# Optimization experiments

Measured on AMD Instinct MI355X. Metric: run time of the kernel, lower is better.

## Reference

```python
import jax, jax.numpy as jnp
import numpy as np

B, N, C, H = 32, 4096, 768, 8
DH = C // H

def setup_inputs() -> dict:
    key = jax.random.key(0)
    k1, k2, k3, k4, k5, k6 = jax.random.split(key, 6)
    s = 0.02
    return {
        "x": jax.random.normal(k1, (B, N, C), dtype=jnp.float32),
        "queries": jax.random.normal(k2, (C,), dtype=jnp.float32),
        "Wq": jax.random.normal(k3, (C, C), dtype=jnp.float32) * s,
        "Wkv": jax.random.normal(k4, (2 * C, C), dtype=jnp.float32) * s,
        "Wproj": jax.random.normal(k5, (C, C), dtype=jnp.float32) * s,
        "bproj": jax.random.normal(k6, (C,), dtype=jnp.float32) * s,
    }

def reference(x, queries, Wq, Wkv, Wproj, bproj):
    # q: single learnable query, shared across batch. torch Linear: y = x @ W^T
    q = (queries @ Wq.T).reshape(H, DH)              # [H, DH]
    kv = jnp.einsum('bnc,ec->bne', x, Wkv)           # [B, N, 2C]
    k, v = jnp.split(kv, 2, axis=-1)
    k = k.reshape(B, N, H, DH)
    v = v.reshape(B, N, H, DH)
    # NOTE: original applies no 1/sqrt(d) scaling
    dots = jnp.einsum('hd,bnhd->bhn', q, k)          # [B, H, N]
    attn = jax.nn.softmax(dots, axis=-1)
    out = jnp.einsum('bhn,bnhd->bhd', attn, v)       # [B, H, DH]
    out = out.reshape(B, 1, C)
    out = jnp.einsum('bnc,ec->bne', out, Wproj) + bproj
    return out                                        # [B, 1, C]
```

## Files before the change

### kernel.cpp

```cpp
#include <hip/hip_runtime.h>

#define B_ 32
#define N_ 4096
#define C_ 768
#define H_ 8
#define DH_ 96
#define TILE 8
#define ROWS 256
#define NT (ROWS / TILE)
#define NCH (N_ / ROWS)
#define TFL (TILE * C_)

struct F3 { float x, y, z; };

#define BARL() do { asm volatile("s_waitcnt lgkmcnt(0)" ::: "memory"); \
                    __builtin_amdgcn_s_barrier(); } while (0)

__global__ __launch_bounds__(256) void k_prep(const float* __restrict__ queries,
    const float* __restrict__ Wq, const float* __restrict__ Wkv,
    float* __restrict__ wqe) {
  __shared__ float qh[DH_];
  const int bid = blockIdx.x;
  const int h = bid / 3, coff = (bid % 3) * 256;
  const int tid = threadIdx.x, lane = tid & 63, wv = tid >> 6;

  float4 q0 = *(const float4*)(queries + lane * 4);
  float4 q1 = *(const float4*)(queries + 256 + lane * 4);
  float4 q2 = *(const float4*)(queries + 512 + lane * 4);
#pragma unroll 4
  for (int j = 0; j < 24; ++j) {
    int d = wv * 24 + j;
    const float* wr = Wq + (size_t)(h * DH_ + d) * C_ + lane * 4;
    float4 w0 = *(const float4*)(wr);
    float4 w1 = *(const float4*)(wr + 256);
    float4 w2 = *(const float4*)(wr + 512);
    float a = w0.x * q0.x;
    a = fmaf(w0.y, q0.y, a); a = fmaf(w0.z, q0.z, a); a = fmaf(w0.w, q0.w, a);
    a = fmaf(w1.x, q1.x, a); a = fmaf(w1.y, q1.y, a);
    a = fmaf(w1.z, q1.z, a); a = fmaf(w1.w, q1.w, a);
    a = fmaf(w2.x, q2.x, a); a = fmaf(w2.y, q2.y, a);
    a = fmaf(w2.z, q2.z, a); a = fmaf(w2.w, q2.w, a);
#pragma unroll
    for (int off = 32; off; off >>= 1) a += __shfl_xor(a, off);
    if (lane == 0) qh[d] = a;
  }
  __syncthreads();

  const int c = coff + tid;
  const float* base = Wkv + (size_t)h * DH_ * C_ + c;
  float a = 0.f;
#pragma unroll 8
  for (int d = 0; d < DH_; ++d)
    a = fmaf(qh[d], base[(size_t)d * C_], a);
  wqe[(size_t)h * C_ + c] = a;
}

__global__ __attribute__((amdgpu_flat_work_group_size(256, 256),
                          amdgpu_waves_per_eu(2, 2))) void k_fused(
    const float* __restrict__ x, const float* __restrict__ wqe,
    float* __restrict__ part, float* __restrict__ sout) {
  extern __shared__ __align__(16) float xdyn[];
  __shared__ __align__(16) float wlds[TILE][H_];
  __shared__ float sden[4][4];

  const int ch = blockIdx.x, b = blockIdx.y;
  const int tid = threadIdx.x, lane = tid & 63, wid = tid >> 6;
  const int rbase = (wid & 1) * 4;
  const int hbase = (wid >> 1) * 4;
  const int col = lane * 4;
  const float* xc = x + ((size_t)b * N_ + (size_t)ch * ROWS) * C_;

  float4 wqv[4][3];
#pragma unroll
  for (int h = 0; h < 4; ++h)
#pragma unroll
    for (int p = 0; p < 3; ++p)
      wqv[h][p] = *(const float4*)(wqe + (size_t)(hbase + h) * C_ + p * 256 + col);

  float acc[H_][3];
#pragma unroll
  for (int h = 0; h < H_; ++h) { acc[h][0] = 0.f; acc[h][1] = 0.f; acc[h][2] = 0.f; }
  float sreg = 0.f;

#define STAGE(BI, T) do {                                                      \
    const float* gt_ = xc + (size_t)(T) * TFL;                                 \
    float* bn_ = xdyn + (size_t)(BI) * TFL;                                    \
    _Pragma("unroll")                                                          \
    for (int j = 0; j < 6; ++j) {                                              \
      int k = wid * 6 + j;                                                     \
      __builtin_amdgcn_global_load_lds(                                        \
        (const __attribute__((address_space(1))) void*)(gt_ + k * 256 + lane * 4), \
        (__attribute__((address_space(3))) void*)(bn_ + k * 256),              \
        16, 0, 0);                                                             \
    }                                                                          \
  } while (0)

  STAGE(0, 0);
  STAGE(1, 1);

  int bi = 0;
  for (int t = 0; t < NT; ++t) {
    if (t < NT - 1) { asm volatile("s_waitcnt vmcnt(6)" ::: "memory"); }
    else           { asm volatile("s_waitcnt vmcnt(0)" ::: "memory"); }
    BARL();
    if (t + 2 < NT) { int nb = bi + 2; if (nb >= 3) nb -= 3; STAGE(nb, t + 2); }
    const float* xb = xdyn + (size_t)bi * TFL;

#pragma unroll
    for (int rr = 0; rr < 4; ++rr) {
      const int r = rbase + rr;
      const float* xr = xb + r * C_ + col;
      float4 xv0 = *(const float4*)(xr);
      float4 xv1 = *(const float4*)(xr + 256);
      float4 xv2 = *(const float4*)(xr + 512);
      float d[4];
#pragma unroll
      for (int h = 0; h < 4; ++h) {
        float a = xv0.x * wqv[h][0].x;
        a = fmaf(xv0.y, wqv[h][0].y, a);
        a = fmaf(xv0.z, wqv[h][0].z, a);
        a = fmaf(xv0.w, wqv[h][0].w, a);
        a = fmaf(xv1.x, wqv[h][1].x, a);
        a = fmaf(xv1.y, wqv[h][1].y, a);
        a = fmaf(xv1.z, wqv[h][1].z, a);
        a = fmaf(xv1.w, wqv[h][1].w, a);
        a = fmaf(xv2.x, wqv[h][2].x, a);
        a = fmaf(xv2.y, wqv[h][2].y, a);
        a = fmaf(xv2.z, wqv[h][2].z, a);
        a = fmaf(xv2.w, wqv[h][2].w, a);
        d[h] = a;
      }
      const int s1 = lane & 1, s2 = lane & 2;
      float A0 = (s1 ? d[1] : d[0]) + __shfl_xor(s1 ? d[0] : d[1], 1);
      float A1 = (s1 ? d[3] : d[2]) + __shfl_xor(s1 ? d[2] : d[3], 1);
      float Q  = (s2 ? A1 : A0) + __shfl_xor(s2 ? A0 : A1, 2);
      Q += __shfl_xor(Q, 4);
      Q += __shfl_xor(Q, 8);
      Q += __shfl_xor(Q, 16);
      Q += __shfl_xor(Q, 32);
      float w = __expf(Q - 20.f);
      if (lane < 4) { wlds[r][hbase + lane] = w; sreg += w; }
    }
    BARL();

    {
      const int c0 = tid * 3;
#pragma unroll
      for (int r = 0; r < TILE; ++r) {
        float4 wA = *(const float4*)(&wlds[r][0]);
        float4 wB = *(const float4*)(&wlds[r][4]);
        F3 xv = *(const F3*)(xb + r * C_ + c0);
        acc[0][0] = fmaf(wA.x, xv.x, acc[0][0]);
        acc[0][1] = fmaf(wA.x, xv.y, acc[0][1]);
        acc[0][2] = fmaf(wA.x, xv.z, acc[0][2]);
        acc[1][0] = fmaf(wA.y, xv.x, acc[1][0]);
        acc[1][1] = fmaf(wA.y, xv.y, acc[1][1]);
        acc[1][2] = fmaf(wA.y, xv.z, acc[1][2]);
        acc[2][0] = fmaf(wA.z, xv.x, acc[2][0]);
        acc[2][1] = fmaf(wA.z, xv.y, acc[2][1]);
        acc[2][2] = fmaf(wA.z, xv.z, acc[2][2]);
        acc[3][0] = fmaf(wA.w, xv.x, acc[3][0]);
        acc[3][1] = fmaf(wA.w, xv.y, acc[3][1]);
        acc[3][2] = fmaf(wA.w, xv.z, acc[3][2]);
        acc[4][0] = fmaf(wB.x, xv.x, acc[4][0]);
        acc[4][1] = fmaf(wB.x, xv.y, acc[4][1]);
        acc[4][2] = fmaf(wB.x, xv.z, acc[4][2]);
        acc[5][0] = fmaf(wB.y, xv.x, acc[5][0]);
        acc[5][1] = fmaf(wB.y, xv.y, acc[5][1]);
        acc[5][2] = fmaf(wB.y, xv.z, acc[5][2]);
        acc[6][0] = fmaf(wB.z, xv.x, acc[6][0]);
        acc[6][1] = fmaf(wB.z, xv.y, acc[6][1]);
        acc[6][2] = fmaf(wB.z, xv.z, acc[6][2]);
        acc[7][0] = fmaf(wB.w, xv.x, acc[7][0]);
        acc[7][1] = fmaf(wB.w, xv.y, acc[7][1]);
        acc[7][2] = fmaf(wB.w, xv.z, acc[7][2]);
      }
    }
    ++bi; if (bi >= 3) bi -= 3;
  }

  {
    const int c0 = tid * 3;
    float* pp = part + ((size_t)(b * NCH + ch) * H_) * C_ + c0;
#pragma unroll
    for (int h = 0; h < H_; ++h) {
      F3 o = { acc[h][0], acc[h][1], acc[h][2] };
      *(F3*)(pp + (size_t)h * C_) = o;
    }
    if (lane < 4) sden[wid][lane] = sreg;
    BARL();
    if (tid < H_) {
      int hh = tid >> 2;
      float den = sden[2 * hh][tid & 3] + sden[2 * hh + 1][tid & 3];
      sout[(size_t)(b * NCH + ch) * H_ + tid] = den;
    }
  }
#undef STAGE
}

__global__ __launch_bounds__(256) void k_combout(
    const float* __restrict__ part, const float* __restrict__ spart,
    const float* __restrict__ Wkv, float* __restrict__ out1) {
  __shared__ __align__(16) float xb[C_];
  const int h = blockIdx.x, b = blockIdx.y;
  const int tid = threadIdx.x, lane = tid & 63, wv = tid >> 6;

  const float* sp = spart + (size_t)b * NCH * H_ + h;
  float den = 0.f;
#pragma unroll
  for (int ch = 0; ch < NCH; ++ch) den += sp[(size_t)ch * H_];
  const float inv = 1.f / den;

  const int c0 = tid * 3;
  const float* pp = part + ((size_t)(b * NCH) * H_ + h) * C_ + c0;
  float a0 = 0.f, a1 = 0.f, a2 = 0.f;
#pragma unroll
  for (int ch = 0; ch < NCH; ++ch) {
    const float* p = pp + (size_t)ch * H_ * C_;
    a0 += p[0]; a1 += p[1]; a2 += p[2];
  }
  xb[c0] = a0 * inv; xb[c0 + 1] = a1 * inv; xb[c0 + 2] = a2 * inv;
  __syncthreads();

  float4 x0 = *(const float4*)(&xb[lane * 4]);
  float4 x1 = *(const float4*)(&xb[256 + lane * 4]);
  float4 x2 = *(const float4*)(&xb[512 + lane * 4]);
#pragma unroll 4
  for (int j = 0; j < 24; ++j) {
    int e = h * DH_ + wv * 24 + j;
    const float* wr = Wkv + (size_t)(C_ + e) * C_ + lane * 4;
    float4 w0 = *(const float4*)(wr);
    float4 w1 = *(const float4*)(wr + 256);
    float4 w2 = *(const float4*)(wr + 512);
    float a = w0.x * x0.x;
    a = fmaf(w0.y, x0.y, a); a = fmaf(w0.z, x0.z, a); a = fmaf(w0.w, x0.w, a);
    a = fmaf(w1.x, x1.x, a); a = fmaf(w1.y, x1.y, a);
    a = fmaf(w1.z, x1.z, a); a = fmaf(w1.w, x1.w, a);
    a = fmaf(w2.x, x2.x, a); a = fmaf(w2.y, x2.y, a);
    a = fmaf(w2.z, x2.z, a); a = fmaf(w2.w, x2.w, a);
#pragma unroll
    for (int off = 32; off; off >>= 1) a += __shfl_xor(a, off);
    if (lane == 0) out1[(size_t)b * C_ + e] = a;
  }
}

__global__ __launch_bounds__(256) void k_proj2(
    const float* __restrict__ out1, const float* __restrict__ Wproj,
    const float* __restrict__ bproj, float* __restrict__ y) {
  __shared__ __align__(16) float xb[C_];
  const int esl = blockIdx.x, b = blockIdx.y;
  const int tid = threadIdx.x, lane = tid & 63, wv = tid >> 6;

  if (tid < 192) ((float4*)xb)[tid] = ((const float4*)(out1 + (size_t)b * C_))[tid];
  __syncthreads();

  float4 x0 = *(const float4*)(&xb[lane * 4]);
  float4 x1 = *(const float4*)(&xb[256 + lane * 4]);
  float4 x2 = *(const float4*)(&xb[512 + lane * 4]);
#pragma unroll 4
  for (int j = 0; j < 24; ++j) {
    int e = esl * DH_ + wv * 24 + j;
    const float* wr = Wproj + (size_t)e * C_ + lane * 4;
    float4 w0 = *(const float4*)(wr);
    float4 w1 = *(const float4*)(wr + 256);
    float4 w2 = *(const float4*)(wr + 512);
    float a = w0.x * x0.x;
    a = fmaf(w0.y, x0.y, a); a = fmaf(w0.z, x0.z, a); a = fmaf(w0.w, x0.w, a);
    a = fmaf(w1.x, x1.x, a); a = fmaf(w1.y, x1.y, a);
    a = fmaf(w1.z, x1.z, a); a = fmaf(w1.w, x1.w, a);
    a = fmaf(w2.x, x2.x, a); a = fmaf(w2.y, x2.y, a);
    a = fmaf(w2.z, x2.z, a); a = fmaf(w2.w, x2.w, a);
#pragma unroll
    for (int off = 32; off; off >>= 1) a += __shfl_xor(a, off);
    if (lane == 0) y[(size_t)b * C_ + e] = a + bproj[e];
  }
}

extern "C" void kernel_launch(void* const* d_in, const int* in_sizes, int n_in,
                              void* d_out, int out_size, void* d_ws, size_t ws_size,
                              hipStream_t stream) {
  const float* x       = (const float*)d_in[0];
  const float* queries = (const float*)d_in[1];
  const float* Wq      = (const float*)d_in[2];
  const float* Wkv     = (const float*)d_in[3];
  const float* Wproj   = (const float*)d_in[4];
  const float* bproj   = (const float*)d_in[5];
  float* y  = (float*)d_out;
  float* ws = (float*)d_ws;

  float* wqe   = ws + 1024;
  float* spart = ws + 8192;
  float* part  = ws + 16384;
  float* out1  = part + (size_t)B_ * NCH * H_ * C_;

  hipLaunchKernelGGL(k_prep,    dim3(24),       dim3(256), 0, stream, queries, Wq, Wkv, wqe);
  hipLaunchKernelGGL(k_fused,   dim3(NCH, B_),  dim3(256),
                     3 * TFL * sizeof(float), stream, x, wqe, part, spart);
  hipLaunchKernelGGL(k_combout, dim3(H_, B_),   dim3(256), 0, stream, part, spart, Wkv, out1);
  hipLaunchKernelGGL(k_proj2,   dim3(H_, B_),   dim3(256), 0, stream, out1, Wproj, bproj, y);
}
```

Measured before the change: 180.1 us.

## Register-prefetch x tiles and compute scores from registers before LDS write

Replaces the triple-buffered global_load_lds pipeline with a register double-buffer: each wave loads its two rows into registers one tile ahead, computes all eight head scores directly from registers, then writes x and weights to a static double-buffered LDS for the weighted accumulation. Each wave now holds all eight head query vectors (96 extra VGPRs) and handles two rows instead of four rows by four heads. This removes one barrier per tile and the LDS read in the score phase, at the cost of much higher register pressure, an extra LDS write pass and only one tile of prefetch depth.

```diff
diff --git a/kernel.cpp b/kernel.cpp
--- a/kernel.cpp
+++ b/kernel.cpp
@@ -59,124 +59,140 @@
                           amdgpu_waves_per_eu(2, 2))) void k_fused(
     const float* __restrict__ x, const float* __restrict__ wqe,
     float* __restrict__ part, float* __restrict__ sout) {
-  extern __shared__ __align__(16) float xdyn[];
-  __shared__ __align__(16) float wlds[TILE][H_];
-  __shared__ float sden[4][4];
+  __shared__ __align__(16) float xsh[2][TFL];
+  __shared__ __align__(16) float wlds[2][TILE][H_];
+  __shared__ float sden[4][H_];
 
   const int ch = blockIdx.x, b = blockIdx.y;
   const int tid = threadIdx.x, lane = tid & 63, wid = tid >> 6;
-  const int rbase = (wid & 1) * 4;
-  const int hbase = (wid >> 1) * 4;
+  const int r0 = wid * 2;
   const int col = lane * 4;
   const float* xc = x + ((size_t)b * N_ + (size_t)ch * ROWS) * C_;
 
-  float4 wqv[4][3];
-#pragma unroll
-  for (int h = 0; h < 4; ++h)
-#pragma unroll
-    for (int p = 0; p < 3; ++p)
-      wqv[h][p] = *(const float4*)(wqe + (size_t)(hbase + h) * C_ + p * 256 + col);
+  float4 wq[3][H_];
+#pragma unroll
+  for (int p = 0; p < 3; ++p)
+#pragma unroll
+    for (int h = 0; h < H_; ++h)
+      wq[p][h] = *(const float4*)(wqe + (size_t)h * C_ + p * 256 + col);
 
   float acc[H_][3];
 #pragma unroll
   for (int h = 0; h < H_; ++h) { acc[h][0] = 0.f; acc[h][1] = 0.f; acc[h][2] = 0.f; }
   float sreg = 0.f;
 
-#define STAGE(BI, T) do {                                                      \
-    const float* gt_ = xc + (size_t)(T) * TFL;                                 \
-    float* bn_ = xdyn + (size_t)(BI) * TFL;                                    \
-    _Pragma("unroll")                                                          \
-    for (int j = 0; j < 6; ++j) {                                              \
-      int k = wid * 6 + j;                                                     \
-      __builtin_amdgcn_global_load_lds(                                        \
-        (const __attribute__((address_space(1))) void*)(gt_ + k * 256 + lane * 4), \
-        (__attribute__((address_space(3))) void*)(bn_ + k * 256),              \
-        16, 0, 0);                                                             \
-    }                                                                          \
+  const int l1 = lane & 1, l2 = (lane >> 1) & 1, l4 = (lane >> 2) & 1;
+
+  float4 stA[6], stB[6];
+
+#define LOADT(DST, T) do {                                                  \
+    const float* gt_ = xc + (size_t)(T) * TFL + (size_t)r0 * C_ + col;      \
+    DST[0] = *(const float4*)(gt_);                                         \
+    DST[1] = *(const float4*)(gt_ + 256);                                   \
+    DST[2] = *(const float4*)(gt_ + 512);                                   \
+    DST[3] = *(const float4*)(gt_ + C_);                                    \
+    DST[4] = *(const float4*)(gt_ + C_ + 256);                              \
+    DST[5] = *(const float4*)(gt_ + C_ + 512);                              \
   } while (0)
 
-  STAGE(0, 0);
-  STAGE(1, 1);
-
-  int bi = 0;
-  for (int t = 0; t < NT; ++t) {
-    if (t < NT - 1) { asm volatile("s_waitcnt vmcnt(6)" ::: "memory"); }
-    else           { asm volatile("s_waitcnt vmcnt(0)" ::: "memory"); }
-    BARL();
-    if (t + 2 < NT) { int nb = bi + 2; if (nb >= 3) nb -= 3; STAGE(nb, t + 2); }
-    const float* xb = xdyn + (size_t)bi * TFL;
-
-#pragma unroll
-    for (int rr = 0; rr < 4; ++rr) {
-      const int r = rbase + rr;
-      const float* xr = xb + r * C_ + col;
-      float4 xv0 = *(const float4*)(xr);
-      float4 xv1 = *(const float4*)(xr + 256);
-      float4 xv2 = *(const float4*)(xr + 512);
-      float d[4];
-#pragma unroll
-      for (int h = 0; h < 4; ++h) {
-        float a = xv0.x * wqv[h][0].x;
-        a = fmaf(xv0.y, wqv[h][0].y, a);
-        a = fmaf(xv0.z, wqv[h][0].z, a);
-        a = fmaf(xv0.w, wqv[h][0].w, a);
-        a = fmaf(xv1.x, wqv[h][1].x, a);
-        a = fmaf(xv1.y, wqv[h][1].y, a);
-        a = fmaf(xv1.z, wqv[h][1].z, a);
-        a = fmaf(xv1.w, wqv[h][1].w, a);
-        a = fmaf(xv2.x, wqv[h][2].x, a);
-        a = fmaf(xv2.y, wqv[h][2].y, a);
-        a = fmaf(xv2.z, wqv[h][2].z, a);
-        a = fmaf(xv2.w, wqv[h][2].w, a);
-        d[h] = a;
-      }
-      const int s1 = lane & 1, s2 = lane & 2;
-      float A0 = (s1 ? d[1] : d[0]) + __shfl_xor(s1 ? d[0] : d[1], 1);
-      float A1 = (s1 ? d[3] : d[2]) + __shfl_xor(s1 ? d[2] : d[3], 1);
-      float Q  = (s2 ? A1 : A0) + __shfl_xor(s2 ? A0 : A1, 2);
-      Q += __shfl_xor(Q, 4);
-      Q += __shfl_xor(Q, 8);
-      Q += __shfl_xor(Q, 16);
-      Q += __shfl_xor(Q, 32);
-      float w = __expf(Q - 20.f);
-      if (lane < 4) { wlds[r][hbase + lane] = w; sreg += w; }
-    }
-    BARL();
-
-    {
-      const int c0 = tid * 3;
-#pragma unroll
-      for (int r = 0; r < TILE; ++r) {
-        float4 wA = *(const float4*)(&wlds[r][0]);
-        float4 wB = *(const float4*)(&wlds[r][4]);
-        F3 xv = *(const F3*)(xb + r * C_ + c0);
-        acc[0][0] = fmaf(wA.x, xv.x, acc[0][0]);
-        acc[0][1] = fmaf(wA.x, xv.y, acc[0][1]);
-        acc[0][2] = fmaf(wA.x, xv.z, acc[0][2]);
-        acc[1][0] = fmaf(wA.y, xv.x, acc[1][0]);
-        acc[1][1] = fmaf(wA.y, xv.y, acc[1][1]);
-        acc[1][2] = fmaf(wA.y, xv.z, acc[1][2]);
-        acc[2][0] = fmaf(wA.z, xv.x, acc[2][0]);
-        acc[2][1] = fmaf(wA.z, xv.y, acc[2][1]);
-        acc[2][2] = fmaf(wA.z, xv.z, acc[2][2]);
-        acc[3][0] = fmaf(wA.w, xv.x, acc[3][0]);
-        acc[3][1] = fmaf(wA.w, xv.y, acc[3][1]);
-        acc[3][2] = fmaf(wA.w, xv.z, acc[3][2]);
-        acc[4][0] = fmaf(wB.x, xv.x, acc[4][0]);
-        acc[4][1] = fmaf(wB.x, xv.y, acc[4][1]);
-        acc[4][2] = fmaf(wB.x, xv.z, acc[4][2]);
-        acc[5][0] = fmaf(wB.y, xv.x, acc[5][0]);
-        acc[5][1] = fmaf(wB.y, xv.y, acc[5][1]);
-        acc[5][2] = fmaf(wB.y, xv.z, acc[5][2]);
-        acc[6][0] = fmaf(wB.z, xv.x, acc[6][0]);
-        acc[6][1] = fmaf(wB.z, xv.y, acc[6][1]);
-        acc[6][2] = fmaf(wB.z, xv.z, acc[6][2]);
-        acc[7][0] = fmaf(wB.w, xv.x, acc[7][0]);
-        acc[7][1] = fmaf(wB.w, xv.y, acc[7][1]);
-        acc[7][2] = fmaf(wB.w, xv.z, acc[7][2]);
-      }
-    }
-    ++bi; if (bi >= 3) bi -= 3;
+#define ROWDOT(V0, V1, V2, WOUT) do {                                       \
+    float d_[H_];                                                           \
+    _Pragma("unroll")                                                       \
+    for (int h = 0; h < H_; ++h) {                                          \
+      float a_ = (V0).x * wq[0][h].x;                                       \
+      a_ = fmaf((V0).y, wq[0][h].y, a_);                                    \
+      a_ = fmaf((V0).z, wq[0][h].z, a_);                                    \
+      a_ = fmaf((V0).w, wq[0][h].w, a_);                                    \
+      a_ = fmaf((V1).x, wq[1][h].x, a_);                                    \
+      a_ = fmaf((V1).y, wq[1][h].y, a_);                                    \
+      a_ = fmaf((V1).z, wq[1][h].z, a_);                                    \
+      a_ = fmaf((V1).w, wq[1][h].w, a_);                                    \
+      a_ = fmaf((V2).x, wq[2][h].x, a_);                                    \
+      a_ = fmaf((V2).y, wq[2][h].y, a_);                                    \
+      a_ = fmaf((V2).z, wq[2][h].z, a_);                                    \
+      a_ = fmaf((V2).w, wq[2][h].w, a_);                                    \
+      d_[h] = a_;                                                           \
+    }                                                                       \
+    float k_, g_;                                                           \
+    k_ = l1 ? d_[1] : d_[0]; g_ = l1 ? d_[0] : d_[1];                       \
+    float q0_ = k_ + __shfl_xor(g_, 1);                                     \
+    k_ = l1 ? d_[3] : d_[2]; g_ = l1 ? d_[2] : d_[3];                       \
+    float q1_ = k_ + __shfl_xor(g_, 1);                                     \
+    k_ = l1 ? d_[5] : d_[4]; g_ = l1 ? d_[4] : d_[5];                       \
+    float q2_ = k_ + __shfl_xor(g_, 1);                                     \
+    k_ = l1 ? d_[7] : d_[6]; g_ = l1 ? d_[6] : d_[7];                       \
+    float q3_ = k_ + __shfl_xor(g_, 1);                                     \
+    k_ = l2 ? q1_ : q0_; g_ = l2 ? q0_ : q1_;                               \
+    float r0_ = k_ + __shfl_xor(g_, 2);                                     \
+    k_ = l2 ? q3_ : q2_; g_ = l2 ? q2_ : q3_;                               \
+    float r1_ = k_ + __shfl_xor(g_, 2);                                     \
+    k_ = l4 ? r1_ : r0_; g_ = l4 ? r0_ : r1_;                               \
+    float t_ = k_ + __shfl_xor(g_, 4);                                      \
+    t_ += __shfl_xor(t_, 8);                                                \
+    t_ += __shfl_xor(t_, 16);                                               \
+    t_ += __shfl_xor(t_, 32);                                               \
+    WOUT = __expf(t_ - 20.f);                                               \
+  } while (0)
+
+#define BODY(T, P, CUR, NXT) do {                                           \
+    if ((T) + 1 < NT) LOADT(NXT, (T) + 1);                                  \
+    if ((T) + 1 < NT) { asm volatile("s_waitcnt vmcnt(6)" ::: "memory"); }  \
+    else              { asm volatile("s_waitcnt vmcnt(0)" ::: "memory"); }  \
+    float wA_, wB_;                                                         \
+    ROWDOT(CUR[0], CUR[1], CUR[2], wA_);                                    \
+    ROWDOT(CUR[3], CUR[4], CUR[5], wB_);                                    \
+    sreg += wA_ + wB_;                                                      \
+    if (lane < H_) {                                                        \
+      wlds[P][r0][lane]     = wA_;                                          \
+      wlds[P][r0 + 1][lane] = wB_;                                          \
+    }                                                                       \
+    { float* bw = &xsh[P][(size_t)r0 * C_];                                 \
+      *(float4*)(bw + col)            = CUR[0];                             \
+      *(float4*)(bw + 256 + col)      = CUR[1];                             \
+      *(float4*)(bw + 512 + col)      = CUR[2];                             \
+      *(float4*)(bw + C_ + col)       = CUR[3];                             \
+      *(float4*)(bw + C_ + 256 + col) = CUR[4];                             \
+      *(float4*)(bw + C_ + 512 + col) = CUR[5];                             \
+    }                                                                       \
+    BARL();                                                                 \
+    { const int c0 = tid * 3;                                               \
+      _Pragma("unroll")                                                     \
+      for (int r = 0; r < TILE; ++r) {                                      \
+        float4 wAv = *(const float4*)(&wlds[P][r][0]);                      \
+        float4 wBv = *(const float4*)(&wlds[P][r][4]);                      \
+        F3 xv = *(const F3*)(&xsh[P][(size_t)r * C_ + c0]);                 \
+        acc[0][0] = fmaf(wAv.x, xv.x, acc[0][0]);                           \
+        acc[0][1] = fmaf(wAv.x, xv.y, acc[0][1]);                           \
+        acc[0][2] = fmaf(wAv.x, xv.z, acc[0][2]);                           \
+        acc[1][0] = fmaf(wAv.y, xv.x, acc[1][0]);                           \
+        acc[1][1] = fmaf(wAv.y, xv.y, acc[1][1]);                           \
+        acc[1][2] = fmaf(wAv.y, xv.z, acc[1][2]);                           \
+        acc[2][0] = fmaf(wAv.z, xv.x, acc[2][0]);                           \
+        acc[2][1] = fmaf(wAv.z, xv.y, acc[2][1]);                           \
+        acc[2][2] = fmaf(wAv.z, xv.z, acc[2][2]);                           \
+        acc[3][0] = fmaf(wAv.w, xv.x, acc[3][0]);                           \
+        acc[3][1] = fmaf(wAv.w, xv.y, acc[3][1]);                           \
+        acc[3][2] = fmaf(wAv.w, xv.z, acc[3][2]);                           \
+        acc[4][0] = fmaf(wBv.x, xv.x, acc[4][0]);                           \
+        acc[4][1] = fmaf(wBv.x, xv.y, acc[4][1]);                           \
+        acc[4][2] = fmaf(wBv.x, xv.z, acc[4][2]);                           \
+        acc[5][0] = fmaf(wBv.y, xv.x, acc[5][0]);                           \
+        acc[5][1] = fmaf(wBv.y, xv.y, acc[5][1]);                           \
+        acc[5][2] = fmaf(wBv.y, xv.z, acc[5][2]);                           \
+        acc[6][0] = fmaf(wBv.z, xv.x, acc[6][0]);                           \
+        acc[6][1] = fmaf(wBv.z, xv.y, acc[6][1]);                           \
+        acc[6][2] = fmaf(wBv.z, xv.z, acc[6][2]);                           \
+        acc[7][0] = fmaf(wBv.w, xv.x, acc[7][0]);                           \
+        acc[7][1] = fmaf(wBv.w, xv.y, acc[7][1]);                           \
+        acc[7][2] = fmaf(wBv.w, xv.z, acc[7][2]);                           \
+      }                                                                     \
+    }                                                                       \
+  } while (0)
+
+  LOADT(stA, 0);
+  for (int t2 = 0; t2 < NT; t2 += 2) {
+    BODY(t2,     0, stA, stB);
+    BODY(t2 + 1, 1, stB, stA);
   }
 
   {
@@ -187,15 +203,16 @@
       F3 o = { acc[h][0], acc[h][1], acc[h][2] };
       *(F3*)(pp + (size_t)h * C_) = o;
     }
-    if (lane < 4) sden[wid][lane] = sreg;
+    if (lane < H_) sden[wid][lane] = sreg;
     BARL();
     if (tid < H_) {
-      int hh = tid >> 2;
-      float den = sden[2 * hh][tid & 3] + sden[2 * hh + 1][tid & 3];
+      float den = sden[0][tid] + sden[1][tid] + sden[2][tid] + sden[3][tid];
       sout[(size_t)(b * NCH + ch) * H_ + tid] = den;
     }
   }
-#undef STAGE
+#undef BODY
+#undef ROWDOT
+#undef LOADT
 }
 
 __global__ __launch_bounds__(256) void k_combout(
@@ -294,8 +311,7 @@
   float* out1  = part + (size_t)B_ * NCH * H_ * C_;
 
   hipLaunchKernelGGL(k_prep,    dim3(24),       dim3(256), 0, stream, queries, Wq, Wkv, wqe);
-  hipLaunchKernelGGL(k_fused,   dim3(NCH, B_),  dim3(256),
-                     3 * TFL * sizeof(float), stream, x, wqe, part, spart);
+  hipLaunchKernelGGL(k_fused,   dim3(NCH, B_),  dim3(256), 0, stream, x, wqe, part, spart);
   hipLaunchKernelGGL(k_combout, dim3(H_, B_),   dim3(256), 0, stream, part, spart, Wkv, out1);
   hipLaunchKernelGGL(k_proj2,   dim3(H_, B_),   dim3(256), 0, stream, out1, Wproj, bproj, y);
 }
```

New measurement: 420.4 us. 134% more time.

## Software-pipeline score and accumulate phases to drop one barrier per tile

Applied to the files above, without the earlier changes.

Restructures the main loop so the weighted-accumulation phase for tile t-1 runs after the score phase of tile t, using double-buffered softmax weights in LDS. This removes the second block barrier per tile. In exchange, global prefetch depth drops from two tiles ahead to one, and every iteration now waits for all outstanding loads (vmcnt(0)), which may expose memory latency.

```diff
diff --git a/kernel.cpp b/kernel.cpp
--- a/kernel.cpp
+++ b/kernel.cpp
@@ -60,7 +60,7 @@
     const float* __restrict__ x, const float* __restrict__ wqe,
     float* __restrict__ part, float* __restrict__ sout) {
   extern __shared__ __align__(16) float xdyn[];
-  __shared__ __align__(16) float wlds[TILE][H_];
+  __shared__ __align__(16) float wlds[2][TILE][H_];
   __shared__ float sden[4][4];
 
   const int ch = blockIdx.x, b = blockIdx.y;
@@ -95,16 +95,49 @@
     }                                                                          \
   } while (0)
 
+#define PHASEC(XB, PC) do {                                                    \
+    const int c0 = tid * 3;                                                    \
+    _Pragma("unroll")                                                          \
+    for (int r = 0; r < TILE; ++r) {                                           \
+      float4 wA = *(const float4*)(&wlds[PC][r][0]);                           \
+      float4 wB = *(const float4*)(&wlds[PC][r][4]);                           \
+      F3 xv = *(const F3*)((XB) + (size_t)r * C_ + c0);                        \
+      acc[0][0] = fmaf(wA.x, xv.x, acc[0][0]);                                 \
+      acc[0][1] = fmaf(wA.x, xv.y, acc[0][1]);                                 \
+      acc[0][2] = fmaf(wA.x, xv.z, acc[0][2]);                                 \
+      acc[1][0] = fmaf(wA.y, xv.x, acc[1][0]);                                 \
+      acc[1][1] = fmaf(wA.y, xv.y, acc[1][1]);                                 \
+      acc[1][2] = fmaf(wA.y, xv.z, acc[1][2]);                                 \
+      acc[2][0] = fmaf(wA.z, xv.x, acc[2][0]);                                 \
+      acc[2][1] = fmaf(wA.z, xv.y, acc[2][1]);                                 \
+      acc[2][2] = fmaf(wA.z, xv.z, acc[2][2]);                                 \
+      acc[3][0] = fmaf(wA.w, xv.x, acc[3][0]);                                 \
+      acc[3][1] = fmaf(wA.w, xv.y, acc[3][1]);                                 \
+      acc[3][2] = fmaf(wA.w, xv.z, acc[3][2]);                                 \
+      acc[4][0] = fmaf(wB.x, xv.x, acc[4][0]);                                 \
+      acc[4][1] = fmaf(wB.x, xv.y, acc[4][1]);                                 \
+      acc[4][2] = fmaf(wB.x, xv.z, acc[4][2]);                                 \
+      acc[5][0] = fmaf(wB.y, xv.x, acc[5][0]);                                 \
+      acc[5][1] = fmaf(wB.y, xv.y, acc[5][1]);                                 \
+      acc[5][2] = fmaf(wB.y, xv.z, acc[5][2]);                                 \
+      acc[6][0] = fmaf(wB.z, xv.x, acc[6][0]);                                 \
+      acc[6][1] = fmaf(wB.z, xv.y, acc[6][1]);                                 \
+      acc[6][2] = fmaf(wB.z, xv.z, acc[6][2]);                                 \
+      acc[7][0] = fmaf(wB.w, xv.x, acc[7][0]);                                 \
+      acc[7][1] = fmaf(wB.w, xv.y, acc[7][1]);                                 \
+      acc[7][2] = fmaf(wB.w, xv.z, acc[7][2]);                                 \
+    }                                                                          \
+  } while (0)
+
   STAGE(0, 0);
-  STAGE(1, 1);
 
   int bi = 0;
   for (int t = 0; t < NT; ++t) {
-    if (t < NT - 1) { asm volatile("s_waitcnt vmcnt(6)" ::: "memory"); }
-    else           { asm volatile("s_waitcnt vmcnt(0)" ::: "memory"); }
+    asm volatile("s_waitcnt vmcnt(0)" ::: "memory");
     BARL();
-    if (t + 2 < NT) { int nb = bi + 2; if (nb >= 3) nb -= 3; STAGE(nb, t + 2); }
+    if (t + 1 < NT) { int nb = bi + 1; if (nb >= 3) nb -= 3; STAGE(nb, t + 1); }
     const float* xb = xdyn + (size_t)bi * TFL;
+    const int P = t & 1;
 
 #pragma unroll
     for (int rr = 0; rr < 4; ++rr) {
@@ -139,44 +172,20 @@
       Q += __shfl_xor(Q, 16);
       Q += __shfl_xor(Q, 32);
       float w = __expf(Q - 20.f);
-      if (lane < 4) { wlds[r][hbase + lane] = w; sreg += w; }
+      if (lane < 4) { wlds[P][r][hbase + lane] = w; sreg += w; }
     }
-    BARL();
-
-    {
-      const int c0 = tid * 3;
-#pragma unroll
-      for (int r = 0; r < TILE; ++r) {
-        float4 wA = *(const float4*)(&wlds[r][0]);
-        float4 wB = *(const float4*)(&wlds[r][4]);
-        F3 xv = *(const F3*)(xb + r * C_ + c0);
-        acc[0][0] = fmaf(wA.x, xv.x, acc[0][0]);
-        acc[0][1] = fmaf(wA.x, xv.y, acc[0][1]);
-        acc[0][2] = fmaf(wA.x, xv.z, acc[0][2]);
-        acc[1][0] = fmaf(wA.y, xv.x, acc[1][0]);
-        acc[1][1] = fmaf(wA.y, xv.y, acc[1][1]);
-        acc[1][2] = fmaf(wA.y, xv.z, acc[1][2]);
-        acc[2][0] = fmaf(wA.z, xv.x, acc[2][0]);
-        acc[2][1] = fmaf(wA.z, xv.y, acc[2][1]);
-        acc[2][2] = fmaf(wA.z, xv.z, acc[2][2]);
-        acc[3][0] = fmaf(wA.w, xv.x, acc[3][0]);
-        acc[3][1] = fmaf(wA.w, xv.y, acc[3][1]);
-        acc[3][2] = fmaf(wA.w, xv.z, acc[3][2]);
-        acc[4][0] = fmaf(wB.x, xv.x, acc[4][0]);
-        acc[4][1] = fmaf(wB.x, xv.y, acc[4][1]);
-        acc[4][2] = fmaf(wB.x, xv.z, acc[4][2]);
-        acc[5][0] = fmaf(wB.y, xv.x, acc[5][0]);
-        acc[5][1] = fmaf(wB.y, xv.y, acc[5][1]);
-        acc[5][2] = fmaf(wB.y, xv.z, acc[5][2]);
-        acc[6][0] = fmaf(wB.z, xv.x, acc[6][0]);
-        acc[6][1] = fmaf(wB.z, xv.y, acc[6][1]);
-        acc[6][2] = fmaf(wB.z, xv.z, acc[6][2]);
-        acc[7][0] = fmaf(wB.w, xv.x, acc[7][0]);
-        acc[7][1] = fmaf(wB.w, xv.y, acc[7][1]);
-        acc[7][2] = fmaf(wB.w, xv.z, acc[7][2]);
-      }
+
+    if (t > 0) {
+      int pb = bi + 2; if (pb >= 3) pb -= 3;
+      PHASEC(xdyn + (size_t)pb * TFL, P ^ 1);
     }
     ++bi; if (bi >= 3) bi -= 3;
+  }
+
+  BARL();
+  {
+    int pb = bi + 2; if (pb >= 3) pb -= 3;
+    PHASEC(xdyn + (size_t)pb * TFL, (NT - 1) & 1);
   }
 
   {
@@ -195,6 +204,7 @@
       sout[(size_t)(b * NCH + ch) * H_ + tid] = den;
     }
   }
+#undef PHASEC
 #undef STAGE
 }
 
```

After: 177.3 us. About the same (-1.5%).
